# Kernel optimization log

Measured on AMD Instinct MI355X. Metric: run time of the kernel, lower is better.

## Reference

```python
import jax, jax.numpy as jnp
import numpy as np

S, B, D = 2048, 2, 1024
H, KV = 16, 4
HD = D // H          # 64
N_REP = H // KV      # 4
EPS = 1e-5
THETA = 10000.0
SCALE = D ** -0.5    # qk_norm_scale = 0.03125 (use_qk_norm path)


def rms_norm(x, w, eps=EPS):
    return x / jnp.sqrt(jnp.mean(x * x, axis=-1, keepdims=True) + eps) * w


def rotate_half(x):
    x1, x2 = jnp.split(x, 2, axis=-1)
    return jnp.concatenate((-x2, x1), axis=-1)


def rope_tables(seq_len, dim, theta=THETA):
    inv_freq = 1.0 / (theta ** (jnp.arange(0, dim, 2, dtype=jnp.float32) / dim))
    t = jnp.arange(seq_len, dtype=jnp.float32)
    freqs = jnp.outer(t, inv_freq)                 # [S, dim/2]
    emb = jnp.concatenate((freqs, freqs), axis=-1)  # [S, dim]
    return jnp.cos(emb), jnp.sin(emb)


def setup_inputs() -> dict:
    key = jax.random.key(0)
    ks = jax.random.split(key, 16)
    s = lambda fan_in: fan_in ** -0.5
    return {
        "x": jax.random.normal(ks[0], (S, B, D), jnp.float32),
        "norm1_w": jnp.ones((D,), jnp.float32),
        "wq": jax.random.normal(ks[1], (D, H * HD), jnp.float32) * s(D),
        "bq": jnp.zeros((H * HD,), jnp.float32),
        "wk": jax.random.normal(ks[2], (D, KV * HD), jnp.float32) * s(D),
        "bk": jnp.zeros((KV * HD,), jnp.float32),
        "wv": jax.random.normal(ks[3], (D, KV * HD), jnp.float32) * s(D),
        "bv": jnp.zeros((KV * HD,), jnp.float32),
        "qn_w": jnp.ones((HD,), jnp.float32),
        "kn_w": jnp.ones((HD,), jnp.float32),
        "wo": jax.random.normal(ks[4], (D, D), jnp.float32) * s(D),
        "bo": jnp.zeros((D,), jnp.float32),
        "norm2_w": jnp.ones((D,), jnp.float32),
        "w1": jax.random.normal(ks[5], (D, 4 * D), jnp.float32) * s(D),
        "b1": jnp.zeros((4 * D,), jnp.float32),
        "w2": jax.random.normal(ks[6], (4 * D, D), jnp.float32) * s(4 * D),
        "b2": jnp.zeros((D,), jnp.float32),
    }


def reference(x, norm1_w, wq, bq, wk, bk, wv, bv, qn_w, kn_w, wo, bo,
              norm2_w, w1, b1, w2, b2):
    # x: [S, B, D] (seq-first, TE convention)
    residual = x
    h = rms_norm(x, norm1_w)
    q = (h @ wq + bq).reshape(S, B, H, HD).transpose(1, 2, 0, 3)    # [B,H,S,HD]
    k = (h @ wk + bk).reshape(S, B, KV, HD).transpose(1, 2, 0, 3)   # [B,KV,S,HD]
    v = (h @ wv + bv).reshape(S, B, KV, HD).transpose(1, 2, 0, 3)
    # GQA: repeat_interleave over head dim
    k = jnp.repeat(k, N_REP, axis=1)  # [B,H,S,HD]
    v = jnp.repeat(v, N_REP, axis=1)
    # per-head QK RMSNorm
    q = rms_norm(q, qn_w)
    k = rms_norm(k, kn_w)
    # RoPE
    cos, sin = rope_tables(S, HD)          # [S,HD] each
    cos = cos[None, None]                  # [1,1,S,HD]
    sin = sin[None, None]
    q = q * cos + rotate_half(q) * sin
    k = k * cos + rotate_half(k) * sin
    # attention with explicit causal mask
    scores = jnp.einsum('bhsd,bhtd->bhst', q, k) * SCALE
    causal = jnp.triu(jnp.ones((S, S), bool), k=1)
    scores = jnp.where(causal, -jnp.inf, scores)
    attn = jax.nn.softmax(scores, axis=-1)
    out = jnp.einsum('bhst,bhtd->bhsd', attn, v)       # [B,H,S,HD]
    out = out.transpose(0, 2, 1, 3).reshape(B, S, D)   # [B,S,D]
    out = out.transpose(1, 0, 2)                       # [S,B,D]
    out = out @ wo + bo
    x = residual + out
    # MLP block (RMSNorm + GELU MLP)
    residual = x
    h2 = rms_norm(x, norm2_w)
    h2 = jax.nn.gelu(h2 @ w1 + b1, approximate=False) @ w2 + b2
    return residual + h2
```

## Files before the change

### kernel.cpp

```cpp
#include <hip/hip_runtime.h>
#include <hip/hip_bf16.h>
#include <math.h>

#define S_LEN 2048
#define BATCH 2
#define DMODEL 1024
#define NH 16
#define NKV 4
#define HDIM 64
#define EPS 1e-5f
#define MROWS (S_LEN*BATCH)
#define QSCALE (0.03125f * 1.44269504088896f)

#define AS1 __attribute__((address_space(1)))
#define AS3 __attribute__((address_space(3)))

typedef __attribute__((ext_vector_type(8))) short bf8_t;
typedef __attribute__((ext_vector_type(4))) float f4_t;
typedef _Float16 __attribute__((ext_vector_type(8))) h8_t;
typedef _Float16 __attribute__((ext_vector_type(4))) h4_t;

#define MFMA16(a,b,c) __builtin_amdgcn_mfma_f32_16x16x16f16(a,b,c,0,0,0)

__device__ __forceinline__ float exp2_fast(float x){ return __builtin_exp2f(x); }

__device__ __forceinline__ unsigned short f2bf(float f){
  __hip_bfloat16 b = __float2bfloat16(f);
  return __builtin_bit_cast(unsigned short, b);
}
__device__ __forceinline__ float bf2f(unsigned short u){
  return __builtin_bit_cast(float, (unsigned)u << 16);
}
__device__ __forceinline__ float gelu_f(float x){
  return 0.5f * x * (1.0f + erff(x * 0.7071067811865475f));
}

__global__ __launch_bounds__(256) void prep_k(const float* __restrict__ wq, const float* __restrict__ wk,
                                              const float* __restrict__ wv, const float* __restrict__ wo,
                                              const float* __restrict__ w1, const float* __restrict__ w2,
                                              __hip_bfloat16* __restrict__ wqkv_t, __hip_bfloat16* __restrict__ wo_t,
                                              __hip_bfloat16* __restrict__ w1_t,   __hip_bfloat16* __restrict__ w2_t,
                                              const float* __restrict__ x, const float* __restrict__ n1w,
                                              __hip_bfloat16* __restrict__ h){
  if (blockIdx.x < 10752){
    __shared__ float t[32][33];
    int b = blockIdx.x;
    const float* src; __hip_bfloat16* dst; int N, stride, nx;
    if (b < 1024)      { src=wq; dst=wqkv_t;               N=1024; stride=1024; nx=32;  }
    else if (b < 1280) { b-=1024; src=wk; dst=wqkv_t+1024*1024; N=256; stride=1024; nx=8; }
    else if (b < 1536) { b-=1280; src=wv; dst=wqkv_t+1280*1024; N=256; stride=1024; nx=8; }
    else if (b < 2560) { b-=1536; src=wo; dst=wo_t;        N=1024; stride=1024; nx=32;  }
    else if (b < 6656) { b-=2560; src=w1; dst=w1_t;        N=4096; stride=1024; nx=128; }
    else               { b-=6656; src=w2; dst=w2_t;        N=1024; stride=4096; nx=32;  }
    int n0 = (b % nx)*32, k0 = (b / nx)*32;
    int tx = threadIdx.x & 31, ty = threadIdx.x >> 5;
    #pragma unroll
    for (int i = 0; i < 4; ++i)
      t[ty*4+i][tx] = src[(size_t)(k0+ty*4+i)*N + n0 + tx];
    __syncthreads();
    #pragma unroll
    for (int i = 0; i < 4; ++i)
      dst[(size_t)(n0+ty*4+i)*stride + k0 + tx] = __float2bfloat16(t[tx][ty*4+i]);
  } else {
    __shared__ float sm[5];
    size_t row = blockIdx.x - 10752;
    const float4* xr = (const float4*)(x + row * DMODEL);
    float4 v = xr[threadIdx.x];
    float ss = v.x*v.x + v.y*v.y + v.z*v.z + v.w*v.w;
    #pragma unroll
    for (int off = 32; off; off >>= 1) ss += __shfl_down(ss, off);
    if ((threadIdx.x & 63) == 0) sm[threadIdx.x >> 6] = ss;
    __syncthreads();
    if (threadIdx.x == 0) sm[4] = rsqrtf((sm[0]+sm[1]+sm[2]+sm[3]) * (1.0f/DMODEL) + EPS);
    __syncthreads();
    float r = sm[4];
    float4 wv4 = ((const float4*)n1w)[threadIdx.x];
    ushort4 ob;
    ob.x = f2bf(v.x*r*wv4.x); ob.y = f2bf(v.y*r*wv4.y);
    ob.z = f2bf(v.z*r*wv4.z); ob.w = f2bf(v.w*r*wv4.w);
    ((ushort4*)(h + row * DMODEL))[threadIdx.x] = ob;
  }
}

template<int EPI, bool DB>
__global__ __launch_bounds__(256) void mgemm_k(const __hip_bfloat16* __restrict__ A,
                                               const __hip_bfloat16* __restrict__ Wt,
                                               const float* __restrict__ bias,
                                               __hip_bfloat16* __restrict__ Cb,
                                               int N, int Kstride, int kLen, int sy){
  __shared__ __align__(16) __hip_bfloat16 As[DB?2:1][8192];
  __shared__ __align__(16) __hip_bfloat16 Bs[DB?2:1][8192];
  const int tid = threadIdx.x;
  const int w = tid >> 6, l = tid & 63;
  const int lr = l & 15, lc = l >> 4;
  const int lr7 = lr & 7;
  const int rrow = l >> 3;
  const int kch  = (l & 7) ^ rrow;

  const unsigned gx = gridDim.x, gy = gridDim.y;
  unsigned hb  = (blockIdx.z * gy + blockIdx.y) * gx + blockIdx.x;
  unsigned xcd = hb & 7u;
  unsigned i   = hb >> 3;
  unsigned cgPerX = (gx * gridDim.z) >> 3;
  unsigned stSz = cgPerX * (unsigned)sy;
  unsigned st  = i / stSz, rr2 = i % stSz;
  unsigned cgl = rr2 % cgPerX, yy = rr2 / cgPerX;
  unsigned byi = st * (unsigned)sy + yy;
  unsigned cg  = xcd * cgPerX + cgl;
  unsigned bxi = cg % gx;
  unsigned bzi = cg / gx;

  const int bm = byi * 128, bn = bxi * 128;
  const int wm = (w >> 1) * 64, wn = (w & 1) * 64;
  const int kOff = bzi * kLen;

  const __hip_bfloat16* Ag = A  + (size_t)(bm + 32*w + rrow)*Kstride + kOff + kch*8;
  const __hip_bfloat16* Bg = Wt + (size_t)(bn + 32*w + rrow)*Kstride + kOff + kch*8;

  f4_t acc[4][4] = {};

  auto stage = [&](int buf, int k0){
    #pragma unroll
    for (int ii = 0; ii < 4; ++ii){
      __builtin_amdgcn_global_load_lds((const AS1 void*)(Ag + (size_t)(8*ii)*Kstride + k0),
                                       (AS3 void*)(&As[buf][w*2048 + ii*512 + l*8]), 16, 0, 0);
      __builtin_amdgcn_global_load_lds((const AS1 void*)(Bg + (size_t)(8*ii)*Kstride + k0),
                                       (AS3 void*)(&Bs[buf][w*2048 + ii*512 + l*8]), 16, 0, 0);
    }
  };

  auto compute = [&](int buf){
    #pragma unroll
    for (int s = 0; s < 2; ++s){
      const int kx = (s*32 + lc*8) ^ (lr7*8);
      bf8_t af[4], bfr[4];
      #pragma unroll
      for (int mi = 0; mi < 4; ++mi)
        af[mi] = *(const bf8_t*)(&As[buf][(wm + mi*16 + lr)*64 + kx]);
      #pragma unroll
      for (int ni = 0; ni < 4; ++ni)
        bfr[ni] = *(const bf8_t*)(&Bs[buf][(wn + ni*16 + lr)*64 + kx]);
      #pragma unroll
      for (int mi = 0; mi < 4; ++mi)
        #pragma unroll
        for (int ni = 0; ni < 4; ++ni)
          acc[mi][ni] = __builtin_amdgcn_mfma_f32_16x16x32_bf16(af[mi], bfr[ni], acc[mi][ni], 0, 0, 0);
    }
  };

  if constexpr (DB){
    const int nt = kLen >> 6;
    stage(0, 0);
    asm volatile("s_waitcnt vmcnt(0)" ::: "memory");
    __builtin_amdgcn_s_barrier();
    int cur = 0;
    for (int t = 0; t < nt; ++t){
      if (t + 1 < nt) stage(cur ^ 1, (t + 1) << 6);
      compute(cur);
      asm volatile("s_waitcnt vmcnt(0)" ::: "memory");
      __builtin_amdgcn_s_barrier();
      cur ^= 1;
    }
  } else {
    for (int k0 = 0; k0 < kLen; k0 += 64){
      __syncthreads();
      stage(0, k0);
      __syncthreads();
      compute(0);
    }
  }

  __hip_bfloat16* Cp = (EPI == 3) ? (Cb + (size_t)bzi * ((size_t)MROWS * N)) : Cb;

  #pragma unroll
  for (int ni = 0; ni < 4; ++ni){
    int col = bn + wn + ni*16 + lr;
    float bb = (EPI == 3) ? 0.0f : bias[col];
    #pragma unroll
    for (int mi = 0; mi < 4; ++mi){
      #pragma unroll
      for (int r = 0; r < 4; ++r){
        int row = bm + wm + mi*16 + lc*4 + r;
        size_t off = (size_t)row * N + col;
        float v = acc[mi][ni][r] + bb;
        if (EPI == 1) Cp[off] = __float2bfloat16(gelu_f(v));
        else          Cp[off] = __float2bfloat16(v);
      }
    }
  }
}

template<int NS>
__global__ __launch_bounds__(256) void reduce_k(const unsigned short* __restrict__ P,
                                                const float* __restrict__ bias,
                                                const float* __restrict__ res,
                                                float* __restrict__ out, int N){
  size_t i = ((size_t)blockIdx.x*256 + threadIdx.x) * 4;
  int col = (int)(i % (size_t)N);
  size_t stride = (size_t)MROWS * N;
  float a0=0,a1=0,a2=0,a3=0;
  #pragma unroll
  for (int p = 0; p < NS; ++p){
    ushort4 u = *(const ushort4*)(P + p*stride + i);
    a0 += bf2f(u.x); a1 += bf2f(u.y); a2 += bf2f(u.z); a3 += bf2f(u.w);
  }
  float4 bb = *(const float4*)(bias + col);
  float4 r4 = *(const float4*)(res + i);
  float4 o = make_float4(a0+bb.x+r4.x, a1+bb.y+r4.y, a2+bb.z+r4.z, a3+bb.w+r4.w);
  *(float4*)(out + i) = o;
}

template<int NS>
__global__ __launch_bounds__(256) void redn_k(const unsigned short* __restrict__ P,
                                              const float* __restrict__ bias,
                                              const float* __restrict__ res,
                                              const float* __restrict__ nw,
                                              float* __restrict__ x1,
                                              __hip_bfloat16* __restrict__ h){
  __shared__ float sm[5];
  size_t row = blockIdx.x;
  size_t i = row * DMODEL + threadIdx.x*4;
  size_t stride = (size_t)MROWS * DMODEL;
  float4 bb = *(const float4*)(bias + threadIdx.x*4);
  float4 r4 = *(const float4*)(res + i);
  float4 v = make_float4(bb.x+r4.x, bb.y+r4.y, bb.z+r4.z, bb.w+r4.w);
  #pragma unroll
  for (int p = 0; p < NS; ++p){
    ushort4 u = *(const ushort4*)(P + p*stride + i);
    v.x += bf2f(u.x); v.y += bf2f(u.y); v.z += bf2f(u.z); v.w += bf2f(u.w);
  }
  *(float4*)(x1 + i) = v;
  float ss = v.x*v.x + v.y*v.y + v.z*v.z + v.w*v.w;
  #pragma unroll
  for (int off = 32; off; off >>= 1) ss += __shfl_down(ss, off);
  if ((threadIdx.x & 63) == 0) sm[threadIdx.x >> 6] = ss;
  __syncthreads();
  if (threadIdx.x == 0) sm[4] = rsqrtf((sm[0]+sm[1]+sm[2]+sm[3]) * (1.0f/DMODEL) + EPS);
  __syncthreads();
  float r = sm[4];
  float4 wv = ((const float4*)nw)[threadIdx.x];
  ushort4 ob;
  ob.x = f2bf(v.x*r*wv.x); ob.y = f2bf(v.y*r*wv.y);
  ob.z = f2bf(v.z*r*wv.z); ob.w = f2bf(v.w*r*wv.w);
  ((ushort4*)(h + row * DMODEL))[threadIdx.x] = ob;
}

__global__ __launch_bounds__(64) void rope2_k(const unsigned short* __restrict__ P,
                                              const float* __restrict__ bq, const float* __restrict__ bk,
                                              const float* __restrict__ qw, const float* __restrict__ kw,
                                              _Float16* __restrict__ qo, _Float16* __restrict__ ko){
  const int s = blockIdx.x;
  const int y = blockIdx.y;
  const int b = y / 20, r0 = y % 20;
  const bool isQ = (r0 < 16);
  const int hh = isQ ? r0 : (r0 - 16);
  const int col0 = isQ ? hh*64 : 1024 + hh*64;
  const int lane = threadIdx.x;
  const size_t pstride = (size_t)MROWS * 1536;
  size_t off = ((size_t)s * BATCH + b) * 1536 + col0 + lane;
  float v = bf2f(P[off]) + bf2f(P[off + pstride])
          + (isQ ? bq[hh*64 + lane] : bk[hh*64 + lane]);
  float ss = v * v;
  #pragma unroll
  for (int m = 32; m; m >>= 1) ss += __shfl_xor(ss, m);
  float rr = rsqrtf(ss * (1.0f/64.0f) + EPS);
  v = v * rr * (isQ ? qw[lane] : kw[lane]);
  int i = lane & 31;
  float invf = powf(10000.0f, -((float)(2*i)) * (1.0f/64.0f));
  float ang = (float)s * invf;
  float c, sn;
  sincosf(ang, &sn, &c);
  float partner = __shfl_xor(v, 32);
  float rh = (lane < 32) ? -partner : partner;
  float o = (v * c + rh * sn) * (isQ ? QSCALE : 1.0f);
  _Float16* outp = isQ ? (qo + (((size_t)b * NH  + hh) * S_LEN + s) * 64 + lane)
                       : (ko + (((size_t)b * NKV + hh) * S_LEN + s) * 64 + lane);
  *outp = (_Float16)o;
}

__global__ __launch_bounds__(256) void vcast_k(const unsigned short* __restrict__ P,
                                               const float* __restrict__ bv,
                                               _Float16* __restrict__ Vt){
  __shared__ float t[64][65];
  const int s0 = blockIdx.x * 64;
  const int bkv = blockIdx.y;
  const int b = bkv >> 2, kv = bkv & 3;
  const int tid = threadIdx.x;
  const size_t pstride = (size_t)MROWS * 1536;
  #pragma unroll
  for (int i = 0; i < 16; ++i){
    int idx = tid + 256*i;
    int sl = idx >> 6, d = idx & 63;
    size_t off = ((size_t)(s0+sl)*BATCH + b)*1536 + 1280 + kv*64 + d;
    t[d][sl] = bf2f(P[off]) + bf2f(P[off + pstride]) + bv[kv*64 + d];
  }
  __syncthreads();
  #pragma unroll
  for (int i = 0; i < 16; ++i){
    int idx = tid + 256*i;
    int d = idx >> 6, sl = idx & 63;
    Vt[((size_t)bkv*64 + d)*S_LEN + s0 + sl] = (_Float16)t[d][sl];
  }
}

__global__ __launch_bounds__(256) void attn2_k(const _Float16* __restrict__ Q,
                                               const _Float16* __restrict__ K,
                                               const _Float16* __restrict__ Vt,
                                               __hip_bfloat16* __restrict__ AO){
  __shared__ __align__(16) _Float16 Ks[8*512];
  __shared__ __align__(16) _Float16 Vs[8*512];
  const int bh = blockIdx.x;
  const int qb = (gridDim.y - 1) - blockIdx.y;
  const int b = bh >> 4, h = bh & 15;
  const int kvh = h >> 2;
  const int tid = threadIdx.x;
  const int w = tid >> 6, l = tid & 63;
  const int lr = l & 15, quad = l >> 4;

  const _Float16* qp = Q + ((size_t)bh * S_LEN + qb*64 + w*16 + lr) * 64;
  h8_t qf0 = *(const h8_t*)(qp + quad*8);
  h8_t qf1 = *(const h8_t*)(qp + 32 + quad*8);

  const _Float16* kbase = K  + (size_t)(b*NKV + kvh) * S_LEN * 64;
  const _Float16* vbase = Vt + (size_t)(b*NKV + kvh) * 64 * S_LEN;

  f4_t Od[4] = {};
  float m_i = -3.0e38f, l_i = 0.0f;

  for (int kt = 0; kt <= qb; ++kt){
    __syncthreads();
    #pragma unroll
    for (int ii = 0; ii < 4; ++ii){
      int i = w*4 + ii;
      if (i < 8){
        int cc = i >> 1, dh = i & 1;
        const _Float16* src = kbase + (size_t)(kt*64 + cc*16 + lr)*64 + dh*32 + quad*8;
        __builtin_amdgcn_global_load_lds((const AS1 void*)src, (AS3 void*)(Ks + i*512), 16, 0, 0);
      } else {
        int j = i - 8;
        int dd = j >> 1, cc32 = j & 1;
        const _Float16* src = vbase + (size_t)(dd*16 + lr)*S_LEN + kt*64 + cc32*32 + quad*8;
        __builtin_amdgcn_global_load_lds((const AS1 void*)src, (AS3 void*)(Vs + j*512), 16, 0, 0);
      }
    }
    __syncthreads();

    const bool diag = (kt == qb);
    f4_t sc[4];
    #pragma unroll
    for (int nc2 = 0; nc2 < 4; ++nc2){
      if (diag && nc2 > w){
        sc[nc2][0] = -1.0e30f; sc[nc2][1] = -1.0e30f;
        sc[nc2][2] = -1.0e30f; sc[nc2][3] = -1.0e30f;
        continue;
      }
      f4_t a = {};
      h8_t k0 = *(const h8_t*)(Ks + (nc2*2+0)*512 + l*8);
      h8_t k1 = *(const h8_t*)(Ks + (nc2*2+1)*512 + l*8);
      a = __builtin_amdgcn_mfma_f32_16x16x32_f16(k0, qf0, a, 0, 0, 0);
      a = __builtin_amdgcn_mfma_f32_16x16x32_f16(k1, qf1, a, 0, 0, 0);
      if (diag && nc2 == w){
        #pragma unroll
        for (int r = 0; r < 4; ++r)
          if (quad*4 + r > lr) a[r] = -1.0e30f;
      }
      sc[nc2] = a;
    }

    float mx = sc[0][0];
    #pragma unroll
    for (int nc2 = 0; nc2 < 4; ++nc2)
      #pragma unroll
      for (int r = 0; r < 4; ++r) mx = fmaxf(mx, sc[nc2][r]);
    mx = fmaxf(mx, __shfl_xor(mx, 16));
    mx = fmaxf(mx, __shfl_xor(mx, 32));
    float nm = fmaxf(mx, m_i);
    float alpha = exp2_fast(m_i - nm);
    m_i = nm;
    float rs = 0.0f;
    h4_t pf[4];
    #pragma unroll
    for (int nc2 = 0; nc2 < 4; ++nc2)
      #pragma unroll
      for (int r = 0; r < 4; ++r){
        float e = exp2_fast(sc[nc2][r] - nm);
        rs += e;
        pf[nc2][r] = (_Float16)e;
      }
    rs += __shfl_xor(rs, 16);
    rs += __shfl_xor(rs, 32);
    l_i = l_i * alpha + rs;
    #pragma unroll
    for (int dd = 0; dd < 4; ++dd)
      #pragma unroll
      for (int r = 0; r < 4; ++r) Od[dd][r] *= alpha;

    #pragma unroll
    for (int dd = 0; dd < 4; ++dd)
      #pragma unroll
      for (int nc2 = 0; nc2 < 4; ++nc2){
        if (diag && nc2 > w) continue;
        h4_t vf = *(const h4_t*)(Vs + (dd*2 + (nc2>>1))*512
                                 + (((nc2&1)*2 + (quad>>1))*16 + lr)*8 + (quad&1)*4);
        Od[dd] = MFMA16(vf, pf[nc2], Od[dd]);
      }
  }

  float inv = 1.0f / l_i;
  #pragma unroll
  for (int dd = 0; dd < 4; ++dd){
    ushort4 w4;
    w4.x = f2bf(Od[dd][0]*inv); w4.y = f2bf(Od[dd][1]*inv);
    w4.z = f2bf(Od[dd][2]*inv); w4.w = f2bf(Od[dd][3]*inv);
    size_t sg = (size_t)qb*64 + w*16 + lr;
    *(ushort4*)(AO + (sg*BATCH + b)*DMODEL + h*64 + dd*16 + quad*4) = w4;
  }
}

extern "C" void kernel_launch(void* const* d_in, const int* in_sizes, int n_in,
                              void* d_out, int out_size, void* d_ws, size_t ws_size,
                              hipStream_t stream){
  const float* x   = (const float*)d_in[0];
  const float* n1w = (const float*)d_in[1];
  const float* wq  = (const float*)d_in[2];
  const float* bq  = (const float*)d_in[3];
  const float* wk  = (const float*)d_in[4];
  const float* bk  = (const float*)d_in[5];
  const float* wv  = (const float*)d_in[6];
  const float* bv  = (const float*)d_in[7];
  const float* qnw = (const float*)d_in[8];
  const float* knw = (const float*)d_in[9];
  const float* wo  = (const float*)d_in[10];
  const float* bo  = (const float*)d_in[11];
  const float* n2w = (const float*)d_in[12];
  const float* w1  = (const float*)d_in[13];
  const float* b1  = (const float*)d_in[14];
  const float* w2  = (const float*)d_in[15];
  const float* b2  = (const float*)d_in[16];
  float* out = (float*)d_out;

  char* p = (char*)d_ws;
  auto carve = [&](size_t bytes)->char*{ char* r = p; p += (bytes + 255) & ~(size_t)255; return r; };
  __hip_bfloat16* h_bf   = (__hip_bfloat16*)carve((size_t)MROWS*DMODEL*2);
  __hip_bfloat16* ao_bf  = (__hip_bfloat16*)carve((size_t)MROWS*DMODEL*2);
  __hip_bfloat16* mid_bf = (__hip_bfloat16*)carve((size_t)MROWS*4096*2);
  __hip_bfloat16* wqkv_t = (__hip_bfloat16*)carve((size_t)1536*1024*2);
  __hip_bfloat16* wo_t   = (__hip_bfloat16*)carve((size_t)1024*1024*2);
  __hip_bfloat16* w1_t   = (__hip_bfloat16*)carve((size_t)4096*1024*2);
  __hip_bfloat16* w2_t   = (__hip_bfloat16*)carve((size_t)1024*4096*2);
  char* scratch = carve((size_t)2*MROWS*1536*2);
  __hip_bfloat16* qkv_p = (__hip_bfloat16*)scratch;
  __hip_bfloat16* ps    = (__hip_bfloat16*)scratch;
  _Float16* q_f  = (_Float16*)carve((size_t)BATCH*NH *S_LEN*64*2);
  _Float16* k_f  = (_Float16*)carve((size_t)BATCH*NKV*S_LEN*64*2);
  _Float16* vt_f = (_Float16*)carve((size_t)BATCH*NKV*64*S_LEN*2);
  float* x1   = (float*)carve((size_t)MROWS*DMODEL*4);

  prep_k<<<10752 + MROWS, 256, 0, stream>>>(wq, wk, wv, wo, w1, w2,
                                            wqkv_t, wo_t, w1_t, w2_t, x, n1w, h_bf);

  mgemm_k<3,true><<<dim3(12, 32, 2), 256, 0, stream>>>(h_bf, wqkv_t, nullptr, qkv_p, 1536, 1024, 512, 8);

  rope2_k<<<dim3(S_LEN, BATCH*20), 64, 0, stream>>>((const unsigned short*)qkv_p, bq, bk, qnw, knw, q_f, k_f);
  vcast_k<<<dim3(S_LEN/64, BATCH*NKV), 256, 0, stream>>>((const unsigned short*)qkv_p, bv, vt_f);
  attn2_k<<<dim3(BATCH*NH, S_LEN/64), 256, 0, stream>>>(q_f, k_f, vt_f, ao_bf);

  mgemm_k<3,true><<<dim3(8, 32, 2), 256, 0, stream>>>(ao_bf, wo_t, nullptr, ps, 1024, 1024, 512, 8);
  redn_k<2><<<MROWS, 256, 0, stream>>>((const unsigned short*)ps, bo, x, n2w, x1, h_bf);

  mgemm_k<1,true><<<dim3(32, 32, 1), 256, 0, stream>>>(h_bf, w1_t, b1, mid_bf, 4096, 1024, 1024, 8);

  mgemm_k<3,false><<<dim3(8, 32, 2), 256, 0, stream>>>(mid_bf, w2_t, nullptr, ps, 1024, 4096, 2048, 4);
  reduce_k<2><<<4096, 256, 0, stream>>>((const unsigned short*)ps, b2, x1, out, 1024);
}
```

Measured before the change: 369.7 us.

## Double-buffer attention K/V LDS tiles and precompute RoPE sin/cos tables

```diff
diff --git a/kernel.cpp b/kernel.cpp
--- a/kernel.cpp
+++ b/kernel.cpp
@@ -41,7 +41,8 @@
                                               __hip_bfloat16* __restrict__ wqkv_t, __hip_bfloat16* __restrict__ wo_t,
                                               __hip_bfloat16* __restrict__ w1_t,   __hip_bfloat16* __restrict__ w2_t,
                                               const float* __restrict__ x, const float* __restrict__ n1w,
-                                              __hip_bfloat16* __restrict__ h){
+                                              __hip_bfloat16* __restrict__ h,
+                                              float* __restrict__ ctab, float* __restrict__ stab){
   if (blockIdx.x < 10752){
     __shared__ float t[32][33];
     int b = blockIdx.x;
@@ -61,7 +62,7 @@
     #pragma unroll
     for (int i = 0; i < 4; ++i)
       dst[(size_t)(n0+ty*4+i)*stride + k0 + tx] = __float2bfloat16(t[tx][ty*4+i]);
-  } else {
+  } else if (blockIdx.x < 10752 + MROWS){
     __shared__ float sm[5];
     size_t row = blockIdx.x - 10752;
     const float4* xr = (const float4*)(x + row * DMODEL);
@@ -79,6 +80,14 @@
     ob.x = f2bf(v.x*r*wv4.x); ob.y = f2bf(v.y*r*wv4.y);
     ob.z = f2bf(v.z*r*wv4.z); ob.w = f2bf(v.w*r*wv4.w);
     ((ushort4*)(h + row * DMODEL))[threadIdx.x] = ob;
+  } else {
+    int idx = (blockIdx.x - (10752 + MROWS))*256 + threadIdx.x;
+    int s = idx >> 5, i = idx & 31;
+    float invf = powf(10000.0f, -((float)(2*i)) * (1.0f/64.0f));
+    float c, sn;
+    sincosf((float)s * invf, &sn, &c);
+    ctab[s*32 + i] = c;
+    stab[s*32 + i] = sn;
   }
 }
 
@@ -248,6 +257,7 @@
 __global__ __launch_bounds__(64) void rope2_k(const unsigned short* __restrict__ P,
                                               const float* __restrict__ bq, const float* __restrict__ bk,
                                               const float* __restrict__ qw, const float* __restrict__ kw,
+                                              const float* __restrict__ ctab, const float* __restrict__ stab,
                                               _Float16* __restrict__ qo, _Float16* __restrict__ ko){
   const int s = blockIdx.x;
   const int y = blockIdx.y;
@@ -266,10 +276,8 @@
   float rr = rsqrtf(ss * (1.0f/64.0f) + EPS);
   v = v * rr * (isQ ? qw[lane] : kw[lane]);
   int i = lane & 31;
-  float invf = powf(10000.0f, -((float)(2*i)) * (1.0f/64.0f));
-  float ang = (float)s * invf;
-  float c, sn;
-  sincosf(ang, &sn, &c);
+  float c  = ctab[s*32 + i];
+  float sn = stab[s*32 + i];
   float partner = __shfl_xor(v, 32);
   float rh = (lane < 32) ? -partner : partner;
   float o = (v * c + rh * sn) * (isQ ? QSCALE : 1.0f);
@@ -307,8 +315,8 @@
                                                const _Float16* __restrict__ K,
                                                const _Float16* __restrict__ Vt,
                                                __hip_bfloat16* __restrict__ AO){
-  __shared__ __align__(16) _Float16 Ks[8*512];
-  __shared__ __align__(16) _Float16 Vs[8*512];
+  __shared__ __align__(16) _Float16 Ks[2][8*512];
+  __shared__ __align__(16) _Float16 Vs[2][8*512];
   const int bh = blockIdx.x;
   const int qb = (gridDim.y - 1) - blockIdx.y;
   const int b = bh >> 4, h = bh & 15;
@@ -327,23 +335,30 @@
   f4_t Od[4] = {};
   float m_i = -3.0e38f, l_i = 0.0f;
 
-  for (int kt = 0; kt <= qb; ++kt){
-    __syncthreads();
+  auto stage = [&](int buf, int kt){
     #pragma unroll
     for (int ii = 0; ii < 4; ++ii){
       int i = w*4 + ii;
       if (i < 8){
         int cc = i >> 1, dh = i & 1;
         const _Float16* src = kbase + (size_t)(kt*64 + cc*16 + lr)*64 + dh*32 + quad*8;
-        __builtin_amdgcn_global_load_lds((const AS1 void*)src, (AS3 void*)(Ks + i*512), 16, 0, 0);
+        __builtin_amdgcn_global_load_lds((const AS1 void*)src, (AS3 void*)(&Ks[buf][i*512] + l*8), 16, 0, 0);
       } else {
         int j = i - 8;
         int dd = j >> 1, cc32 = j & 1;
         const _Float16* src = vbase + (size_t)(dd*16 + lr)*S_LEN + kt*64 + cc32*32 + quad*8;
-        __builtin_amdgcn_global_load_lds((const AS1 void*)src, (AS3 void*)(Vs + j*512), 16, 0, 0);
-      }
-    }
-    __syncthreads();
+        __builtin_amdgcn_global_load_lds((const AS1 void*)src, (AS3 void*)(&Vs[buf][j*512] + l*8), 16, 0, 0);
+      }
+    }
+  };
+
+  stage(0, 0);
+  asm volatile("s_waitcnt vmcnt(0)" ::: "memory");
+  __builtin_amdgcn_s_barrier();
+  int cur = 0;
+
+  for (int kt = 0; kt <= qb; ++kt){
+    if (kt < qb) stage(cur ^ 1, kt + 1);
 
     const bool diag = (kt == qb);
     f4_t sc[4];
@@ -355,8 +370,8 @@
         continue;
       }
       f4_t a = {};
-      h8_t k0 = *(const h8_t*)(Ks + (nc2*2+0)*512 + l*8);
-      h8_t k1 = *(const h8_t*)(Ks + (nc2*2+1)*512 + l*8);
+      h8_t k0 = *(const h8_t*)(&Ks[cur][(nc2*2+0)*512] + l*8);
+      h8_t k1 = *(const h8_t*)(&Ks[cur][(nc2*2+1)*512] + l*8);
       a = __builtin_amdgcn_mfma_f32_16x16x32_f16(k0, qf0, a, 0, 0, 0);
       a = __builtin_amdgcn_mfma_f32_16x16x32_f16(k1, qf1, a, 0, 0, 0);
       if (diag && nc2 == w){
@@ -400,10 +415,14 @@
       #pragma unroll
       for (int nc2 = 0; nc2 < 4; ++nc2){
         if (diag && nc2 > w) continue;
-        h4_t vf = *(const h4_t*)(Vs + (dd*2 + (nc2>>1))*512
+        h4_t vf = *(const h4_t*)(&Vs[cur][(dd*2 + (nc2>>1))*512]
                                  + (((nc2&1)*2 + (quad>>1))*16 + lr)*8 + (quad&1)*4);
         Od[dd] = MFMA16(vf, pf[nc2], Od[dd]);
       }
+
+    asm volatile("s_waitcnt vmcnt(0)" ::: "memory");
+    __builtin_amdgcn_s_barrier();
+    cur ^= 1;
   }
 
   float inv = 1.0f / l_i;
@@ -455,13 +474,16 @@
   _Float16* k_f  = (_Float16*)carve((size_t)BATCH*NKV*S_LEN*64*2);
   _Float16* vt_f = (_Float16*)carve((size_t)BATCH*NKV*64*S_LEN*2);
   float* x1   = (float*)carve((size_t)MROWS*DMODEL*4);
-
-  prep_k<<<10752 + MROWS, 256, 0, stream>>>(wq, wk, wv, wo, w1, w2,
-                                            wqkv_t, wo_t, w1_t, w2_t, x, n1w, h_bf);
+  float* ctab = (float*)carve((size_t)S_LEN*32*4);
+  float* stab = (float*)carve((size_t)S_LEN*32*4);
+
+  prep_k<<<10752 + MROWS + 256, 256, 0, stream>>>(wq, wk, wv, wo, w1, w2,
+                                                  wqkv_t, wo_t, w1_t, w2_t, x, n1w, h_bf,
+                                                  ctab, stab);
 
   mgemm_k<3,true><<<dim3(12, 32, 2), 256, 0, stream>>>(h_bf, wqkv_t, nullptr, qkv_p, 1536, 1024, 512, 8);
 
-  rope2_k<<<dim3(S_LEN, BATCH*20), 64, 0, stream>>>((const unsigned short*)qkv_p, bq, bk, qnw, knw, q_f, k_f);
+  rope2_k<<<dim3(S_LEN, BATCH*20), 64, 0, stream>>>((const unsigned short*)qkv_p, bq, bk, qnw, knw, ctab, stab, q_f, k_f);
   vcast_k<<<dim3(S_LEN/64, BATCH*NKV), 256, 0, stream>>>((const unsigned short*)qkv_p, bv, vt_f);
   attn2_k<<<dim3(BATCH*NH, S_LEN/64), 256, 0, stream>>>(q_f, k_f, vt_f, ao_bf);
 
```

Result: faster. 353.5 us (-4.4%).
